# Kernel optimization log

Measured on AMD Instinct MI355X. Metric: run time of the kernel, lower is better.

The kernel has to match this reference:

```python
import jax, jax.numpy as jnp
import numpy as np

B, S, L, T = 32, 512, 20, 16
E, H, D = 300, 128, 128
V = 50000
SEG = S // T


def _gru_dir(x, Wi, Wh, bi, bh, reverse):
    """One direction of torch-style GRU. x: (B,S,E). Returns (outs (B,S,H), h_final (B,H))."""
    xs = jnp.swapaxes(x, 0, 1)  # (S,B,E)
    h0 = jnp.zeros((x.shape[0], H), x.dtype)

    def step(h, x_t):
        gi = x_t @ Wi.T + bi          # (B,3H) gates order: r,z,n (torch)
        gh = h @ Wh.T + bh
        r = jax.nn.sigmoid(gi[:, :H] + gh[:, :H])
        z = jax.nn.sigmoid(gi[:, H:2 * H] + gh[:, H:2 * H])
        n = jnp.tanh(gi[:, 2 * H:] + r * gh[:, 2 * H:])
        h_new = (1.0 - z) * n + z * h
        return h_new, h_new

    hN, hs = jax.lax.scan(step, h0, xs, reverse=reverse)
    return jnp.swapaxes(hs, 0, 1), hN


def setup_inputs() -> dict:
    key = jax.random.key(0)
    ks = jax.random.split(key, 16)
    word_ids = jax.random.randint(ks[0], (B, S, L), 0, V, dtype=jnp.int32)
    # contiguous, full-coverage topic segments, 1-based boundaries (as in the torch code)
    starts = jnp.tile(jnp.arange(T, dtype=jnp.int32) * SEG + 1, (B, 1))
    ends = jnp.tile((jnp.arange(T, dtype=jnp.int32) + 1) * SEG, (B, 1))
    sent2topic = jnp.tile((jnp.arange(S, dtype=jnp.int32) // SEG), (B, 1))
    sc = 0.08
    return {
        "word_ids": word_ids, "starts": starts, "ends": ends, "sent2topic": sent2topic,
        "embed_table": jax.random.normal(ks[1], (V, E), jnp.float32) * 0.6,
        "Wi_f": jax.random.normal(ks[2], (3 * H, E), jnp.float32) * sc,
        "Wh_f": jax.random.normal(ks[3], (3 * H, H), jnp.float32) * sc,
        "bi_f": jax.random.normal(ks[4], (3 * H,), jnp.float32) * sc,
        "bh_f": jax.random.normal(ks[5], (3 * H,), jnp.float32) * sc,
        "Wi_b": jax.random.normal(ks[6], (3 * H, E), jnp.float32) * sc,
        "Wh_b": jax.random.normal(ks[7], (3 * H, H), jnp.float32) * sc,
        "bi_b": jax.random.normal(ks[8], (3 * H,), jnp.float32) * sc,
        "bh_b": jax.random.normal(ks[9], (3 * H,), jnp.float32) * sc,
        "W_att": jax.random.normal(ks[10], (4 * H, 4 * H), jnp.float32) * 0.05,
        "v_att": jax.random.normal(ks[11], (4 * H, 1), jnp.float32) * 0.05,
        "W1": jax.random.normal(ks[12], (D, 4 * H), jnp.float32) * 0.05,
        "b1": jax.random.normal(ks[13], (D,), jnp.float32) * 0.05,
        "W2": jax.random.normal(ks[14], (1, D), jnp.float32) * 0.05,
        "b2": jax.random.normal(ks[15], (1,), jnp.float32) * 0.05,
    }


def reference(word_ids, starts, ends, sent2topic, embed_table,
              Wi_f, Wh_f, bi_f, bh_f, Wi_b, Wh_b, bi_b, bh_b,
              W_att, v_att, W1, b1, W2, b2):
    # --- sent_encoder: mean of word embeddings per sentence ---
    sent = jnp.take(embed_table, word_ids, axis=0).mean(axis=2)  # (B,S,E)
    # --- doc_encoder: bidirectional GRU ---
    out_f, h_f = _gru_dir(sent, Wi_f, Wh_f, bi_f, bh_f, reverse=False)
    out_b, h_b = _gru_dir(sent, Wi_b, Wh_b, bi_b, bh_b, reverse=True)
    sent_rep = jnp.concatenate([out_f, out_b], axis=-1)          # (B,S,2H)
    # faithful to torch: hidden (2,B,H).view(B,2H)
    hidden = jnp.stack([h_f, h_b], axis=0)
    doc_rep = hidden.reshape(B, 2 * H)
    doc_rep = jnp.broadcast_to(doc_rep[None], (S, B, 2 * H)).swapaxes(0, 1)  # (B,S,2H)
    # --- topic_rep: boundary diffs (padded index i == 1-based sentence i) ---
    padded = jnp.pad(sent_rep, ((0, 0), (1, 1), (0, 0)))          # (B,S+2,2H)
    g = lambda idx: jnp.take_along_axis(padded, idx[:, :, None], axis=1)  # (B,T,2H)
    fwd_diff = g(ends)[..., :H] - g(starts - 1)[..., :H]
    bwd_diff = g(starts)[..., H:] - g(ends + 1)[..., H:]
    topic_mat = jnp.concatenate([fwd_diff, bwd_diff], axis=-1)   # (B,T,2H)
    topic_rep = jnp.take_along_axis(topic_mat, sent2topic[:, :, None], axis=1)  # (B,S,2H)
    # --- decoder ---
    cat_ds = jnp.concatenate([doc_rep, sent_rep], axis=-1)       # (B,S,4H)
    cat_ts = jnp.concatenate([topic_rep, sent_rep], axis=-1)
    doc_scores = jnp.tanh(cat_ds @ W_att) @ v_att                # (B,S,1)
    topic_scores = jnp.tanh(cat_ts @ W_att) @ v_att
    sum_scores = doc_scores + topic_scores
    doc_w = doc_scores / sum_scores
    topic_w = topic_scores / sum_scores
    context = doc_w * doc_rep + topic_w * topic_rep
    inp = jnp.concatenate([sent_rep, context], axis=-1)          # (B,S,4H)
    h = jax.nn.relu(inp @ W1.T + b1)                             # dropout=eval identity
    logits = (h @ W2.T + b2).squeeze(-1)                         # (B,S)
    return logits
```

## Files before the change

kernel.cpp:

```cpp
#include <hip/hip_runtime.h>


#define LDS_BARRIER() do {                                   \
    asm volatile("s_waitcnt lgkmcnt(0)" ::: "memory");       \
    __builtin_amdgcn_s_barrier();                            \
    asm volatile("" ::: "memory");                           \
  } while (0)

__global__ __launch_bounds__(128) void k_sent_mean(
    const int* __restrict__ wid, const float* __restrict__ emb,
    float* __restrict__ sent)
{
  const int bs = blockIdx.x;
  const int tid = threadIdx.x;
  const int* w = wid + (size_t)bs * 20;
  float a0 = 0.f, a1 = 0.f, a2 = 0.f;
  for (int l = 0; l < 20; ++l) {
    const float* row = emb + (size_t)w[l] * 300;
    a0 += row[tid];
    a1 += row[tid + 128];
    if (tid < 44) a2 += row[tid + 256];
  }
  const float inv = 1.0f / 20.0f;
  float* o = sent + (size_t)bs * 300;
  o[tid] = a0 * inv;
  o[tid + 128] = a1 * inv;
  if (tid < 44) o[tid + 256] = a2 * inv;
}

template<bool BT, int ACT>
__global__ __launch_bounds__(256) void k_gemm(
    const int M, const int N, const int K,
    const float* __restrict__ A, const int lda,
    const float* __restrict__ Bm, const int ldb,
    float* __restrict__ C, const int ldc,
    const float* __restrict__ bias)
{
  (void)N;
  __shared__ float As[64][68];
  __shared__ float Bs[64][68];
  const int tid = threadIdx.x;
  const int m0 = blockIdx.x * 64;
  const int n0 = blockIdx.y * 64;
  const int tx = tid & 15;
  const int ty = tid >> 4;
  float acc[4][4] = {};

  for (int kc = 0; kc < K; kc += 64) {
    const int kb = (K - kc < 64) ? (K - kc) : 64;
    #pragma unroll
    for (int r = 0; r < 4; ++r) {
      const int m = r * 16 + ty;
      const int k4 = tx * 4;
      float4 v = make_float4(0.f, 0.f, 0.f, 0.f);
      if (m0 + m < M) {
        const float* ap = A + (size_t)(m0 + m) * lda + kc;
        if (k4 + 4 <= kb) {
          v = *(const float4*)(ap + k4);
        } else {
          float t0 = (k4 + 0 < kb) ? ap[k4 + 0] : 0.f;
          float t1 = (k4 + 1 < kb) ? ap[k4 + 1] : 0.f;
          float t2 = (k4 + 2 < kb) ? ap[k4 + 2] : 0.f;
          float t3 = (k4 + 3 < kb) ? ap[k4 + 3] : 0.f;
          v = make_float4(t0, t1, t2, t3);
        }
      }
      *(float4*)&As[m][k4] = v;
    }
    if (BT) {
      #pragma unroll
      for (int r = 0; r < 4; ++r) {
        const int n = r * 16 + ty;
        const int k4 = tx * 4;
        float4 v = make_float4(0.f, 0.f, 0.f, 0.f);
        const float* bp = Bm + (size_t)(n0 + n) * ldb + kc;
        if (k4 + 4 <= kb) {
          v = *(const float4*)(bp + k4);
        } else {
          float t0 = (k4 + 0 < kb) ? bp[k4 + 0] : 0.f;
          float t1 = (k4 + 1 < kb) ? bp[k4 + 1] : 0.f;
          float t2 = (k4 + 2 < kb) ? bp[k4 + 2] : 0.f;
          float t3 = (k4 + 3 < kb) ? bp[k4 + 3] : 0.f;
          v = make_float4(t0, t1, t2, t3);
        }
        Bs[k4 + 0][n] = v.x;
        Bs[k4 + 1][n] = v.y;
        Bs[k4 + 2][n] = v.z;
        Bs[k4 + 3][n] = v.w;
      }
    } else {
      #pragma unroll
      for (int r = 0; r < 4; ++r) {
        const int kk = r * 16 + ty;
        const int n4 = tx * 4;
        float4 v = make_float4(0.f, 0.f, 0.f, 0.f);
        if (kk < kb) v = *(const float4*)(Bm + (size_t)(kc + kk) * ldb + n0 + n4);
        *(float4*)&Bs[kk][n4] = v;
      }
    }
    __syncthreads();
    #pragma unroll 4
    for (int kk = 0; kk < kb; ++kk) {
      const float4 bv = *(const float4*)&Bs[kk][tx * 4];
      #pragma unroll
      for (int i = 0; i < 4; ++i) {
        const float a = As[ty * 4 + i][kk];
        acc[i][0] = fmaf(a, bv.x, acc[i][0]);
        acc[i][1] = fmaf(a, bv.y, acc[i][1]);
        acc[i][2] = fmaf(a, bv.z, acc[i][2]);
        acc[i][3] = fmaf(a, bv.w, acc[i][3]);
      }
    }
    __syncthreads();
  }

  float bv4[4] = {0.f, 0.f, 0.f, 0.f};
  if (bias != nullptr) {
    #pragma unroll
    for (int j = 0; j < 4; ++j) bv4[j] = bias[n0 + tx * 4 + j];
  }
  #pragma unroll
  for (int i = 0; i < 4; ++i) {
    const int m = m0 + ty * 4 + i;
    if (m < M) {
      float4 o;
      o.x = acc[i][0] + bv4[0];
      o.y = acc[i][1] + bv4[1];
      o.z = acc[i][2] + bv4[2];
      o.w = acc[i][3] + bv4[3];
      if (ACT == 1) {
        o.x = fmaxf(o.x, 0.f); o.y = fmaxf(o.y, 0.f);
        o.z = fmaxf(o.z, 0.f); o.w = fmaxf(o.w, 0.f);
      }
      *(float4*)&C[(size_t)m * ldc + n0 + tx * 4] = o;
    }
  }
}

__global__ __launch_bounds__(768, 3) void k_gru(
    const float* __restrict__ gi_f, const float* __restrict__ gi_b,
    const float* __restrict__ Wh_f, const float* __restrict__ Wh_b,
    const float* __restrict__ bh_f, const float* __restrict__ bh_b,
    float* __restrict__ srep, float* __restrict__ hfin)
{
  const int dir = blockIdx.x & 1;
  const int b = blockIdx.x >> 1;
  const float* gi = (dir ? gi_b : gi_f) + (size_t)b * 512 * 384;
  const float* Wh = dir ? Wh_b : Wh_f;
  const float* bh = dir ? bh_b : bh_f;

  const int tid = threadIdx.x;
  const int half = (tid >= 384) ? 1 : 0;
  const int t = tid - half * 384;

  __shared__ __align__(16) float hlds[128];
  __shared__ float part[2][384];
  __shared__ __align__(16) float gis[2][32 * 384];

  float4 w[16];
  const float* wrow = Wh + (size_t)t * 128 + half * 64;
  #pragma unroll
  for (int kk = 0; kk < 16; ++kk) w[kk] = *(const float4*)(wrow + kk * 4);
  const float bh_t = half ? 0.f : bh[t];

  {
    const int lo0 = dir ? 480 : 0;
    const float4* g4 = (const float4*)gi + lo0 * 96;
    float4* l4 = (float4*)gis[0];
    #pragma unroll
    for (int j = 0; j < 4; ++j) l4[j * 768 + tid] = g4[j * 768 + tid];
  }
  if (tid < 128) hlds[tid] = 0.f;
  LDS_BARRIER();

  const float4* h4 = (const float4*)hlds + half * 16;
  float4 stg[4];

  for (int c = 0; c < 16; ++c) {
    const int buf = c & 1;
    const int lo = dir ? (480 - 32 * c) : (32 * c);
    if (c < 15) {
      const int lon = dir ? (480 - 32 * (c + 1)) : (32 * (c + 1));
      const float4* g4 = (const float4*)gi + lon * 96;
      #pragma unroll
      for (int j = 0; j < 4; ++j) stg[j] = g4[j * 768 + tid];
    }

    for (int i = 0; i < 32; ++i) {
      const int sloc = dir ? (31 - i) : i;
      const int seq = lo + sloc;

      float a0 = bh_t, a1 = 0.f, a2 = 0.f, a3 = 0.f;
      #pragma unroll
      for (int kk = 0; kk < 16; ++kk) {
        const float4 hv = h4[kk];
        a0 = fmaf(w[kk].x, hv.x, a0);
        a1 = fmaf(w[kk].y, hv.y, a1);
        a2 = fmaf(w[kk].z, hv.z, a2);
        a3 = fmaf(w[kk].w, hv.w, a3);
      }
      part[half][t] = (a0 + a1) + (a2 + a3);
      LDS_BARRIER();

      if (tid < 128) {
        const float* grow = &gis[buf][sloc * 384];
        const float ghr = part[0][tid]       + part[1][tid];
        const float ghz = part[0][tid + 128] + part[1][tid + 128];
        const float ghn = part[0][tid + 256] + part[1][tid + 256];
        const float gir = grow[tid];
        const float giz = grow[tid + 128];
        const float gin = grow[tid + 256];
        const float r = 1.f / (1.f + expf(-(gir + ghr)));
        const float z = 1.f / (1.f + expf(-(giz + ghz)));
        const float n = tanhf(gin + r * ghn);
        const float hnew = (1.f - z) * n + z * hlds[tid];
        hlds[tid] = hnew;
        srep[((size_t)(b * 512 + seq)) * 256 + dir * 128 + tid] = hnew;
      }
      LDS_BARRIER();
    }

    if (c < 15) {
      float4* l4 = (float4*)gis[buf ^ 1];
      #pragma unroll
      for (int j = 0; j < 4; ++j) l4[j * 768 + tid] = stg[j];
      LDS_BARRIER();
    }
  }
  if (tid < 128) hfin[(size_t)dir * 4096 + (size_t)b * 128 + tid] = hlds[tid];
}

__global__ __launch_bounds__(256) void k_topic(
    const int* __restrict__ starts, const int* __restrict__ ends,
    const float* __restrict__ srep, float* __restrict__ tmat)
{
  const int bt = blockIdx.x;
  const int b = bt >> 4;
  const int st = starts[bt], en = ends[bt];
  const int j = threadIdx.x;
  float v;
  if (j < 128) {
    const float a = (en >= 1 && en <= 512) ? srep[((size_t)(b * 512 + en - 1)) * 256 + j] : 0.f;
    const float c = (st - 1 >= 1 && st - 1 <= 512) ? srep[((size_t)(b * 512 + st - 2)) * 256 + j] : 0.f;
    v = a - c;
  } else {
    const float a = (st >= 1 && st <= 512) ? srep[((size_t)(b * 512 + st - 1)) * 256 + j] : 0.f;
    const float c = (en + 1 >= 1 && en + 1 <= 512) ? srep[((size_t)(b * 512 + en)) * 256 + j] : 0.f;
    v = a - c;
  }
  tmat[(size_t)bt * 256 + j] = v;
}

__global__ __launch_bounds__(256) void k_scores(
    const float* spart, const float* __restrict__ docp, const float* __restrict__ topp,
    const float* __restrict__ v_att, const float* __restrict__ srep,
    const float* __restrict__ docrep, const float* __restrict__ tmat,
    const int* __restrict__ s2t, float* inp)
{
  const int bs = blockIdx.x;
  const int b = bs >> 9;
  const int tid = threadIdx.x;
  const int tp = s2t[bs];
  const float* sp = spart + (size_t)bs * 512;
  const float* dp = docp + (size_t)b * 512;
  const float* tq = topp + ((size_t)(b * 16 + tp)) * 512;
  float ds = 0.f, ts = 0.f;
  #pragma unroll
  for (int r = 0; r < 2; ++r) {
    const int o = tid + r * 256;
    const float s0 = sp[o], v = v_att[o];
    ds += tanhf(s0 + dp[o]) * v;
    ts += tanhf(s0 + tq[o]) * v;
  }
  #pragma unroll
  for (int off = 32; off; off >>= 1) {
    ds += __shfl_down(ds, off);
    ts += __shfl_down(ts, off);
  }
  __shared__ float rds[4], rts[4], wsh[2];
  const int wv = tid >> 6, ln = tid & 63;
  if (ln == 0) { rds[wv] = ds; rts[wv] = ts; }
  __syncthreads();
  if (tid == 0) {
    const float D = rds[0] + rds[1] + rds[2] + rds[3];
    const float T = rts[0] + rts[1] + rts[2] + rts[3];
    const float sum = D + T;
    wsh[0] = D / sum;
    wsh[1] = T / sum;
  }
  __syncthreads();
  const float dw = wsh[0], tw = wsh[1];
  const float sr = srep[(size_t)bs * 256 + tid];
  const float ctx = dw * docrep[(size_t)b * 256 + tid]
                  + tw * tmat[((size_t)(b * 16 + tp)) * 256 + tid];
  float* op = inp + (size_t)bs * 512;
  op[tid] = sr;
  op[256 + tid] = ctx;
}

__global__ __launch_bounds__(64) void k_logits(
    const float* __restrict__ hbuf, const float* __restrict__ W2,
    const float* __restrict__ b2, float* __restrict__ out)
{
  const int bs = blockIdx.x;
  const int ln = threadIdx.x;
  const float* h = hbuf + (size_t)bs * 128;
  float a = fmaf(h[ln], W2[ln], h[ln + 64] * W2[ln + 64]);
  #pragma unroll
  for (int off = 32; off; off >>= 1) a += __shfl_down(a, off);
  if (ln == 0) out[bs] = a + b2[0];
}

extern "C" void kernel_launch(void* const* d_in, const int* in_sizes, int n_in,
                              void* d_out, int out_size, void* d_ws, size_t ws_size,
                              hipStream_t stream)
{
  (void)in_sizes; (void)n_in; (void)out_size;

  const int*   word_ids = (const int*)d_in[0];
  const int*   starts   = (const int*)d_in[1];
  const int*   ends     = (const int*)d_in[2];
  const int*   s2t      = (const int*)d_in[3];
  const float* emb      = (const float*)d_in[4];
  const float* Wi_f     = (const float*)d_in[5];
  const float* Wh_f     = (const float*)d_in[6];
  const float* bi_f     = (const float*)d_in[7];
  const float* bh_f     = (const float*)d_in[8];
  const float* Wi_b     = (const float*)d_in[9];
  const float* Wh_b     = (const float*)d_in[10];
  const float* bi_b     = (const float*)d_in[11];
  const float* bh_b     = (const float*)d_in[12];
  const float* W_att    = (const float*)d_in[13];
  const float* v_att    = (const float*)d_in[14];
  const float* W1       = (const float*)d_in[15];
  const float* b1       = (const float*)d_in[16];
  const float* W2       = (const float*)d_in[17];
  const float* b2       = (const float*)d_in[18];
  float* out = (float*)d_out;

  char* ws = (char*)d_ws;
  if (ws_size < 88440832u) return;
  float* sent  = (float*)(ws + 0);
  float* gi_f  = (float*)(ws + 19660800);
  float* gi_b  = (float*)(ws + 44826624);
  float* srep  = (float*)(ws + 69992448);
  float* hfin  = (float*)(ws + 86769664);
  float* tmat  = (float*)(ws + 86802432);
  float* docp  = (float*)(ws + 87326720);
  float* topp  = (float*)(ws + 87392256);
  float* spart = (float*)(ws + 19660800);
  float* hbuf  = (float*)(ws + 0);

  k_sent_mean<<<16384, 128, 0, stream>>>(word_ids, emb, sent);
  k_gemm<true, 0><<<dim3(256, 6), 256, 0, stream>>>(16384, 384, 300, sent, 300, Wi_f, 300, gi_f, 384, bi_f);
  k_gemm<true, 0><<<dim3(256, 6), 256, 0, stream>>>(16384, 384, 300, sent, 300, Wi_b, 300, gi_b, 384, bi_b);
  k_gru<<<64, 768, 0, stream>>>(gi_f, gi_b, Wh_f, Wh_b, bh_f, bh_b, srep, hfin);
  k_topic<<<512, 256, 0, stream>>>(starts, ends, srep, tmat);
  k_gemm<false, 0><<<dim3(256, 8), 256, 0, stream>>>(16384, 512, 256, srep, 256, W_att + 256 * 512, 512, spart, 512, nullptr);
  k_gemm<false, 0><<<dim3(1, 8),   256, 0, stream>>>(32,    512, 256, hfin, 256, W_att,            512, docp,  512, nullptr);
  k_gemm<false, 0><<<dim3(8, 8),   256, 0, stream>>>(512,   512, 256, tmat, 256, W_att,            512, topp,  512, nullptr);
  k_scores<<<16384, 256, 0, stream>>>(spart, docp, topp, v_att, srep, hfin, tmat, s2t, spart);
  k_gemm<true, 1><<<dim3(256, 2), 256, 0, stream>>>(16384, 128, 512, spart, 512, W1, 512, hbuf, 128, b1);
  k_logits<<<16384, 64, 0, stream>>>(hbuf, W2, b2, out);
}
```

Before: 863.4 us.

## Shrink GRU block to 256 threads with three gate rows per thread

The recurrent GRU kernel drops from 768 to 256 threads per block. Each thread now holds three rows of Wh (a half-K slice of each) in registers, 192 floats in total, so the block spans four waves instead of twelve. Fewer waves should make the two barriers on every sequential step cheaper, and each thread gets more independent FMAs to hide latency. The hidden state is also carried in a register rather than reread from LDS, and the partial sums are interleaved so the gate thread can read them as float2. The cost is heavy register pressure, which risks spilling, and more gi staging loads per thread.

```diff
diff --git a/kernel.cpp b/kernel.cpp
--- a/kernel.cpp
+++ b/kernel.cpp
@@ -137,7 +137,7 @@
   }
 }
 
-__global__ __launch_bounds__(768, 3) void k_gru(
+__global__ __launch_bounds__(256, 1) void k_gru(
     const float* __restrict__ gi_f, const float* __restrict__ gi_b,
     const float* __restrict__ Wh_f, const float* __restrict__ Wh_b,
     const float* __restrict__ bh_f, const float* __restrict__ bh_b,
@@ -150,72 +150,98 @@
   const float* bh = dir ? bh_b : bh_f;
 
   const int tid = threadIdx.x;
-  const int half = (tid >= 384) ? 1 : 0;
-  const int t = tid - half * 384;
+  const int wv = tid >> 6;
+  const int ln = tid & 63;
+  const int kh = wv & 1;
+  const int rg = wv >> 1;
+  const int r0 = rg * 192 + ln;
 
   __shared__ __align__(16) float hlds[128];
-  __shared__ float part[2][384];
+  __shared__ __align__(8)  float part2[384 * 2];
   __shared__ __align__(16) float gis[2][32 * 384];
 
-  float4 w[16];
-  const float* wrow = Wh + (size_t)t * 128 + half * 64;
-  #pragma unroll
-  for (int kk = 0; kk < 16; ++kk) w[kk] = *(const float4*)(wrow + kk * 4);
-  const float bh_t = half ? 0.f : bh[t];
+  float4 w0[16], w1[16], w2[16];
+  {
+    const float* p = Wh + (size_t)r0 * 128 + kh * 64;
+    #pragma unroll
+    for (int kk = 0; kk < 16; ++kk) w0[kk] = *(const float4*)(p + kk * 4);
+    p += 64 * 128;
+    #pragma unroll
+    for (int kk = 0; kk < 16; ++kk) w1[kk] = *(const float4*)(p + kk * 4);
+    p += 64 * 128;
+    #pragma unroll
+    for (int kk = 0; kk < 16; ++kk) w2[kk] = *(const float4*)(p + kk * 4);
+  }
+  const float bh0 = kh ? 0.f : bh[r0];
+  const float bh1 = kh ? 0.f : bh[r0 + 64];
+  const float bh2 = kh ? 0.f : bh[r0 + 128];
 
   {
     const int lo0 = dir ? 480 : 0;
-    const float4* g4 = (const float4*)gi + lo0 * 96;
+    const float4* g4 = (const float4*)(gi + (size_t)lo0 * 384);
     float4* l4 = (float4*)gis[0];
     #pragma unroll
-    for (int j = 0; j < 4; ++j) l4[j * 768 + tid] = g4[j * 768 + tid];
-  }
+    for (int j = 0; j < 12; ++j) l4[j * 256 + tid] = g4[j * 256 + tid];
+  }
+  float hreg = 0.f;
   if (tid < 128) hlds[tid] = 0.f;
   LDS_BARRIER();
 
-  const float4* h4 = (const float4*)hlds + half * 16;
-  float4 stg[4];
+  const float4* h4 = (const float4*)hlds + kh * 16;
+  float4 stg[12];
 
   for (int c = 0; c < 16; ++c) {
     const int buf = c & 1;
     const int lo = dir ? (480 - 32 * c) : (32 * c);
     if (c < 15) {
       const int lon = dir ? (480 - 32 * (c + 1)) : (32 * (c + 1));
-      const float4* g4 = (const float4*)gi + lon * 96;
-      #pragma unroll
-      for (int j = 0; j < 4; ++j) stg[j] = g4[j * 768 + tid];
+      const float4* g4 = (const float4*)(gi + (size_t)lon * 384);
+      #pragma unroll
+      for (int j = 0; j < 12; ++j) stg[j] = g4[j * 256 + tid];
     }
 
     for (int i = 0; i < 32; ++i) {
       const int sloc = dir ? (31 - i) : i;
       const int seq = lo + sloc;
 
-      float a0 = bh_t, a1 = 0.f, a2 = 0.f, a3 = 0.f;
+      float4 A0 = {0.f, 0.f, 0.f, 0.f};
+      float4 A1 = {0.f, 0.f, 0.f, 0.f};
+      float4 A2 = {0.f, 0.f, 0.f, 0.f};
       #pragma unroll
       for (int kk = 0; kk < 16; ++kk) {
         const float4 hv = h4[kk];
-        a0 = fmaf(w[kk].x, hv.x, a0);
-        a1 = fmaf(w[kk].y, hv.y, a1);
-        a2 = fmaf(w[kk].z, hv.z, a2);
-        a3 = fmaf(w[kk].w, hv.w, a3);
-      }
-      part[half][t] = (a0 + a1) + (a2 + a3);
+        A0.x = fmaf(w0[kk].x, hv.x, A0.x);
+        A0.y = fmaf(w0[kk].y, hv.y, A0.y);
+        A0.z = fmaf(w0[kk].z, hv.z, A0.z);
+        A0.w = fmaf(w0[kk].w, hv.w, A0.w);
+        A1.x = fmaf(w1[kk].x, hv.x, A1.x);
+        A1.y = fmaf(w1[kk].y, hv.y, A1.y);
+        A1.z = fmaf(w1[kk].z, hv.z, A1.z);
+        A1.w = fmaf(w1[kk].w, hv.w, A1.w);
+        A2.x = fmaf(w2[kk].x, hv.x, A2.x);
+        A2.y = fmaf(w2[kk].y, hv.y, A2.y);
+        A2.z = fmaf(w2[kk].z, hv.z, A2.z);
+        A2.w = fmaf(w2[kk].w, hv.w, A2.w);
+      }
+      part2[r0 * 2 + kh]         = (A0.x + A0.y) + (A0.z + A0.w) + bh0;
+      part2[(r0 + 64) * 2 + kh]  = (A1.x + A1.y) + (A1.z + A1.w) + bh1;
+      part2[(r0 + 128) * 2 + kh] = (A2.x + A2.y) + (A2.z + A2.w) + bh2;
       LDS_BARRIER();
 
       if (tid < 128) {
         const float* grow = &gis[buf][sloc * 384];
-        const float ghr = part[0][tid]       + part[1][tid];
-        const float ghz = part[0][tid + 128] + part[1][tid + 128];
-        const float ghn = part[0][tid + 256] + part[1][tid + 256];
+        const float2 pr = *(const float2*)&part2[tid * 2];
+        const float2 pz = *(const float2*)&part2[(tid + 128) * 2];
+        const float2 pn = *(const float2*)&part2[(tid + 256) * 2];
         const float gir = grow[tid];
         const float giz = grow[tid + 128];
         const float gin = grow[tid + 256];
-        const float r = 1.f / (1.f + expf(-(gir + ghr)));
-        const float z = 1.f / (1.f + expf(-(giz + ghz)));
-        const float n = tanhf(gin + r * ghn);
-        const float hnew = (1.f - z) * n + z * hlds[tid];
-        hlds[tid] = hnew;
-        srep[((size_t)(b * 512 + seq)) * 256 + dir * 128 + tid] = hnew;
+        const float r = 1.f / (1.f + expf(-(gir + (pr.x + pr.y))));
+        const float z = 1.f / (1.f + expf(-(giz + (pz.x + pz.y))));
+        const float n = tanhf(gin + r * (pn.x + pn.y));
+        hreg = (1.f - z) * n + z * hreg;
+        hlds[tid] = hreg;
+        srep[((size_t)(b * 512 + seq)) * 256 + dir * 128 + tid] = hreg;
       }
       LDS_BARRIER();
     }
@@ -223,11 +249,11 @@
     if (c < 15) {
       float4* l4 = (float4*)gis[buf ^ 1];
       #pragma unroll
-      for (int j = 0; j < 4; ++j) l4[j * 768 + tid] = stg[j];
+      for (int j = 0; j < 12; ++j) l4[j * 256 + tid] = stg[j];
       LDS_BARRIER();
     }
   }
-  if (tid < 128) hfin[(size_t)dir * 4096 + (size_t)b * 128 + tid] = hlds[tid];
+  if (tid < 128) hfin[(size_t)dir * 4096 + (size_t)b * 128 + tid] = hreg;
 }
 
 __global__ __launch_bounds__(256) void k_topic(
@@ -354,7 +380,7 @@
   k_sent_mean<<<16384, 128, 0, stream>>>(word_ids, emb, sent);
   k_gemm<true, 0><<<dim3(256, 6), 256, 0, stream>>>(16384, 384, 300, sent, 300, Wi_f, 300, gi_f, 384, bi_f);
   k_gemm<true, 0><<<dim3(256, 6), 256, 0, stream>>>(16384, 384, 300, sent, 300, Wi_b, 300, gi_b, 384, bi_b);
-  k_gru<<<64, 768, 0, stream>>>(gi_f, gi_b, Wh_f, Wh_b, bh_f, bh_b, srep, hfin);
+  k_gru<<<64, 256, 0, stream>>>(gi_f, gi_b, Wh_f, Wh_b, bh_f, bh_b, srep, hfin);
   k_topic<<<512, 256, 0, stream>>>(starts, ends, srep, tmat);
   k_gemm<false, 0><<<dim3(256, 8), 256, 0, stream>>>(16384, 512, 256, srep, 256, W_att + 256 * 512, 512, spart, 512, nullptr);
   k_gemm<false, 0><<<dim3(1, 8),   256, 0, stream>>>(32,    512, 256, hfin, 256, W_att,            512, docp,  512, nullptr);
```

Result: slower. 885.3 us (+2.5%).

## Split GRU recurrent matvec 8-way over K with 1024 threads and fast gate math

Applied to the files above, without the earlier changes.

The recurrent GRU kernel now runs 1024 threads per block. Each wave handles a 16-wide K slice for three gate rows, with 8 partial sums reduced in LDS, where before each thread covered half of one row's K. This shortens the serial FMA chain per timestep. The Wh weights are re-read from global/cache every substep into alternating register sets instead of being held in registers for the whole kernel, the hidden state lives in a register, and sigmoid/tanh use fast exp/divide with clamping. The risks are extra per-step cache traffic for the weight reloads, a heavier 8-way reduction, and slight precision loss in the gate math.

```diff
diff --git a/kernel.cpp b/kernel.cpp
--- a/kernel.cpp
+++ b/kernel.cpp
@@ -137,7 +137,7 @@
   }
 }
 
-__global__ __launch_bounds__(768, 3) void k_gru(
+__global__ __launch_bounds__(1024, 4) void k_gru(
     const float* __restrict__ gi_f, const float* __restrict__ gi_b,
     const float* __restrict__ Wh_f, const float* __restrict__ Wh_b,
     const float* __restrict__ bh_f, const float* __restrict__ bh_b,
@@ -150,84 +150,125 @@
   const float* bh = dir ? bh_b : bh_f;
 
   const int tid = threadIdx.x;
-  const int half = (tid >= 384) ? 1 : 0;
-  const int t = tid - half * 384;
+  const int wv = tid >> 6;
+  const int ln = tid & 63;
+  const int kq = wv & 7;
+  const int rg = wv >> 3;
+  const int r0 = rg * 192 + ln;
 
   __shared__ __align__(16) float hlds[128];
-  __shared__ float part[2][384];
+  __shared__ float partl[8 * 384];
   __shared__ __align__(16) float gis[2][32 * 384];
 
-  float4 w[16];
-  const float* wrow = Wh + (size_t)t * 128 + half * 64;
+  const float4* w4r0 = (const float4*)(Wh + (size_t)r0 * 128 + kq * 16);
+  const float4* w4r1 = (const float4*)(Wh + (size_t)(r0 + 64) * 128 + kq * 16);
+  const float4* w4r2 = (const float4*)(Wh + (size_t)(r0 + 128) * 128 + kq * 16);
+
+  const float bh0 = (kq == 0) ? bh[r0] : 0.f;
+  const float bh1 = (kq == 0) ? bh[r0 + 64] : 0.f;
+  const float bh2 = (kq == 0) ? bh[r0 + 128] : 0.f;
+
+  float4 wA[12], wB[12];
   #pragma unroll
-  for (int kk = 0; kk < 16; ++kk) w[kk] = *(const float4*)(wrow + kk * 4);
-  const float bh_t = half ? 0.f : bh[t];
+  for (int j = 0; j < 4; ++j) {
+    wA[j] = w4r0[j]; wA[4 + j] = w4r1[j]; wA[8 + j] = w4r2[j];
+  }
 
   {
     const int lo0 = dir ? 480 : 0;
-    const float4* g4 = (const float4*)gi + lo0 * 96;
+    const float4* g4 = (const float4*)(gi + (size_t)lo0 * 384);
     float4* l4 = (float4*)gis[0];
     #pragma unroll
-    for (int j = 0; j < 4; ++j) l4[j * 768 + tid] = g4[j * 768 + tid];
-  }
+    for (int j = 0; j < 3; ++j) l4[j * 1024 + tid] = g4[j * 1024 + tid];
+  }
+  float hreg = 0.f;
   if (tid < 128) hlds[tid] = 0.f;
   LDS_BARRIER();
 
-  const float4* h4 = (const float4*)hlds + half * 16;
-  float4 stg[4];
+  const float4* h4q = (const float4*)hlds + kq * 4;
+  float4 stg[3];
+
+#define GRU_SUBSTEP(CUR, OTH, IEXPR)                                          \
+  {                                                                           \
+    const int sloc = dir ? (31 - (IEXPR)) : (IEXPR);                          \
+    const int seq = lo + sloc;                                                \
+    _Pragma("unroll")                                                         \
+    for (int j = 0; j < 4; ++j) {                                             \
+      OTH[j] = w4r0[j]; OTH[4 + j] = w4r1[j]; OTH[8 + j] = w4r2[j];           \
+    }                                                                         \
+    float4 A0 = {0.f, 0.f, 0.f, 0.f};                                         \
+    float4 A1 = {0.f, 0.f, 0.f, 0.f};                                         \
+    float4 A2 = {0.f, 0.f, 0.f, 0.f};                                         \
+    _Pragma("unroll")                                                         \
+    for (int j = 0; j < 4; ++j) {                                             \
+      const float4 hv = h4q[j];                                               \
+      A0.x = fmaf(CUR[j].x, hv.x, A0.x);                                      \
+      A0.y = fmaf(CUR[j].y, hv.y, A0.y);                                      \
+      A0.z = fmaf(CUR[j].z, hv.z, A0.z);                                      \
+      A0.w = fmaf(CUR[j].w, hv.w, A0.w);                                      \
+      A1.x = fmaf(CUR[4 + j].x, hv.x, A1.x);                                  \
+      A1.y = fmaf(CUR[4 + j].y, hv.y, A1.y);                                  \
+      A1.z = fmaf(CUR[4 + j].z, hv.z, A1.z);                                  \
+      A1.w = fmaf(CUR[4 + j].w, hv.w, A1.w);                                  \
+      A2.x = fmaf(CUR[8 + j].x, hv.x, A2.x);                                  \
+      A2.y = fmaf(CUR[8 + j].y, hv.y, A2.y);                                  \
+      A2.z = fmaf(CUR[8 + j].z, hv.z, A2.z);                                  \
+      A2.w = fmaf(CUR[8 + j].w, hv.w, A2.w);                                  \
+    }                                                                         \
+    partl[kq * 384 + r0]       = (A0.x + A0.y) + (A0.z + A0.w) + bh0;         \
+    partl[kq * 384 + r0 + 64]  = (A1.x + A1.y) + (A1.z + A1.w) + bh1;         \
+    partl[kq * 384 + r0 + 128] = (A2.x + A2.y) + (A2.z + A2.w) + bh2;         \
+    LDS_BARRIER();                                                            \
+    if (tid < 128) {                                                          \
+      const float* grow = &gis[buf][sloc * 384];                              \
+      float ghr = 0.f, ghz = 0.f, ghn = 0.f;                                  \
+      _Pragma("unroll")                                                       \
+      for (int q = 0; q < 8; ++q) {                                           \
+        ghr += partl[q * 384 + tid];                                          \
+        ghz += partl[q * 384 + tid + 128];                                    \
+        ghn += partl[q * 384 + tid + 256];                                    \
+      }                                                                       \
+      const float gir = grow[tid];                                            \
+      const float giz = grow[tid + 128];                                      \
+      const float gin = grow[tid + 256];                                      \
+      const float r = __fdividef(1.f, 1.f + __expf(-(gir + ghr)));            \
+      const float z = __fdividef(1.f, 1.f + __expf(-(giz + ghz)));            \
+      float an = gin + r * ghn;                                               \
+      an = fminf(fmaxf(an, -15.f), 15.f);                                     \
+      const float t = __expf(2.f * an);                                       \
+      const float n = __fdividef(t - 1.f, t + 1.f);                           \
+      hreg = (1.f - z) * n + z * hreg;                                        \
+      hlds[tid] = hreg;                                                       \
+      srep[((size_t)(b * 512 + seq)) * 256 + dir * 128 + tid] = hreg;         \
+    }                                                                         \
+    LDS_BARRIER();                                                            \
+  }
 
   for (int c = 0; c < 16; ++c) {
     const int buf = c & 1;
     const int lo = dir ? (480 - 32 * c) : (32 * c);
     if (c < 15) {
       const int lon = dir ? (480 - 32 * (c + 1)) : (32 * (c + 1));
-      const float4* g4 = (const float4*)gi + lon * 96;
+      const float4* g4 = (const float4*)(gi + (size_t)lon * 384);
       #pragma unroll
-      for (int j = 0; j < 4; ++j) stg[j] = g4[j * 768 + tid];
-    }
-
-    for (int i = 0; i < 32; ++i) {
-      const int sloc = dir ? (31 - i) : i;
-      const int seq = lo + sloc;
-
-      float a0 = bh_t, a1 = 0.f, a2 = 0.f, a3 = 0.f;
-      #pragma unroll
-      for (int kk = 0; kk < 16; ++kk) {
-        const float4 hv = h4[kk];
-        a0 = fmaf(w[kk].x, hv.x, a0);
-        a1 = fmaf(w[kk].y, hv.y, a1);
-        a2 = fmaf(w[kk].z, hv.z, a2);
-        a3 = fmaf(w[kk].w, hv.w, a3);
-      }
-      part[half][t] = (a0 + a1) + (a2 + a3);
-      LDS_BARRIER();
-
-      if (tid < 128) {
-        const float* grow = &gis[buf][sloc * 384];
-        const float ghr = part[0][tid]       + part[1][tid];
-        const float ghz = part[0][tid + 128] + part[1][tid + 128];
-        const float ghn = part[0][tid + 256] + part[1][tid + 256];
-        const float gir = grow[tid];
-        const float giz = grow[tid + 128];
-        const float gin = grow[tid + 256];
-        const float r = 1.f / (1.f + expf(-(gir + ghr)));
-        const float z = 1.f / (1.f + expf(-(giz + ghz)));
-        const float n = tanhf(gin + r * ghn);
-        const float hnew = (1.f - z) * n + z * hlds[tid];
-        hlds[tid] = hnew;
-        srep[((size_t)(b * 512 + seq)) * 256 + dir * 128 + tid] = hnew;
-      }
-      LDS_BARRIER();
+      for (int j = 0; j < 3; ++j) stg[j] = g4[j * 1024 + tid];
+    }
+
+    for (int i = 0; i < 32; i += 2) {
+      GRU_SUBSTEP(wA, wB, i);
+      GRU_SUBSTEP(wB, wA, i + 1);
     }
 
     if (c < 15) {
       float4* l4 = (float4*)gis[buf ^ 1];
       #pragma unroll
-      for (int j = 0; j < 4; ++j) l4[j * 768 + tid] = stg[j];
+      for (int j = 0; j < 3; ++j) l4[j * 1024 + tid] = stg[j];
       LDS_BARRIER();
     }
   }
-  if (tid < 128) hfin[(size_t)dir * 4096 + (size_t)b * 128 + tid] = hlds[tid];
+#undef GRU_SUBSTEP
+
+  if (tid < 128) hfin[(size_t)dir * 4096 + (size_t)b * 128 + tid] = hreg;
 }
 
 __global__ __launch_bounds__(256) void k_topic(
@@ -354,7 +395,7 @@
   k_sent_mean<<<16384, 128, 0, stream>>>(word_ids, emb, sent);
   k_gemm<true, 0><<<dim3(256, 6), 256, 0, stream>>>(16384, 384, 300, sent, 300, Wi_f, 300, gi_f, 384, bi_f);
   k_gemm<true, 0><<<dim3(256, 6), 256, 0, stream>>>(16384, 384, 300, sent, 300, Wi_b, 300, gi_b, 384, bi_b);
-  k_gru<<<64, 768, 0, stream>>>(gi_f, gi_b, Wh_f, Wh_b, bh_f, bh_b, srep, hfin);
+  k_gru<<<64, 1024, 0, stream>>>(gi_f, gi_b, Wh_f, Wh_b, bh_f, bh_b, srep, hfin);
   k_topic<<<512, 256, 0, stream>>>(starts, ends, srep, tmat);
   k_gemm<false, 0><<<dim3(256, 8), 256, 0, stream>>>(16384, 512, 256, srep, 256, W_att + 256 * 512, 512, spart, 512, nullptr);
   k_gemm<false, 0><<<dim3(1, 8),   256, 0, stream>>>(32,    512, 256, hfin, 256, W_att,            512, docp,  512, nullptr);
```

Result: slower. 2.141 ms (+148.0%).
